# Performance work log

Hardware: AMD Instinct MI355X
Metric: run time of the kernel (lower is better)

Reference implementation:

```python
import jax, jax.numpy as jnp
import numpy as np

N_ITERS = 1000  # hardcoded in the original module
EPS = 1e-6


def setup_inputs() -> dict:
    key = jax.random.key(0)
    k1, k2 = jax.random.split(key)
    embeds = jax.random.normal(k1, (30000, 64), dtype=jnp.float32)
    # torch does t.rand(...) inside forward; we hoist it here for determinism
    init_centroids = jax.random.uniform(k2, (500, 64), dtype=jnp.float32)
    return {"embeds": embeds, "init_centroids": init_centroids}


def reference(embeds, init_centroids):
    N, D = embeds.shape
    K = init_centroids.shape[0]
    # ||e||^2 is loop-invariant; squared L2 distance expanded as
    # ||e||^2 - 2 e.c + ||c||^2 (same math as (e-c)^2.sum(-1), no [N,K,D] blowup)
    e_sq = jnp.sum(embeds * embeds, axis=1)  # [N]
    ones = jnp.ones((N, 1), dtype=embeds.dtype)

    def step(carry, _):
        cents, _, _ = carry
        c_sq = jnp.sum(cents * cents, axis=1)  # [K]
        dists = e_sq[:, None] - 2.0 * (embeds @ cents.T) + c_sq[None, :]  # [N,K]
        idxs = jnp.argmin(dists, axis=1)  # [N] int32
        sums = jax.ops.segment_sum(embeds, idxs, num_segments=K)  # [K,D]
        counts = jax.ops.segment_sum(ones, idxs, num_segments=K)  # [K,1]
        new_cents = sums / (counts + EPS)
        return (new_cents, idxs, counts), None

    init = (init_centroids,
            jnp.zeros((N,), dtype=jnp.int32),
            jnp.zeros((K, 1), dtype=embeds.dtype))
    (centroids, idxs, clust_nums), _ = jax.lax.scan(step, init, None, length=N_ITERS)
    return centroids, idxs, clust_nums
```

## Files before the change

kernel.cpp:

```cpp
#include <hip/hip_runtime.h>
#include <math.h>

#define N_PTS   30000
#define DIM     64
#define K_C     500
#define K_PAD   512
#define N_ITERS 1000

#define GRID 256
#define BLK  512

#define TM    128
#define NTM   235

#define FPSCALE 262144.0f
#define INV_FPSCALE (1.0 / 262144.0)

#define SMEM_BYTES (DIM * TM * 4 + DIM * K_PAD * 4)

#define BAR_STRIDE 32
#define BAR_REL_OFF (GRID * BAR_STRIDE)

__device__ __forceinline__ void gridbar(int* bar, int n) {
  __syncthreads();
  if (blockIdx.x == 0) {
    const int t = threadIdx.x;
    if (t >= 1 && t < GRID) {
      while (__hip_atomic_load(&bar[t * BAR_STRIDE], __ATOMIC_RELAXED,
                               __HIP_MEMORY_SCOPE_AGENT) < n)
        __builtin_amdgcn_s_sleep(2);
      __builtin_amdgcn_fence(__ATOMIC_ACQUIRE, "agent");
    }
    __syncthreads();
    if (t == 0)
      __hip_atomic_store(&bar[BAR_REL_OFF], n, __ATOMIC_RELEASE,
                         __HIP_MEMORY_SCOPE_AGENT);
  } else {
    if (threadIdx.x == 0) {
      __hip_atomic_store(&bar[blockIdx.x * BAR_STRIDE], n, __ATOMIC_RELEASE,
                         __HIP_MEMORY_SCOPE_AGENT);
      while (__hip_atomic_load(&bar[BAR_REL_OFF], __ATOMIC_RELAXED,
                               __HIP_MEMORY_SCOPE_AGENT) < n)
        __builtin_amdgcn_s_sleep(2);
      __builtin_amdgcn_fence(__ATOMIC_ACQUIRE, "agent");
    }
    __syncthreads();
  }
}

__global__ __launch_bounds__(BLK, 2)
void k_persist(const float* __restrict__ embeds,
               const float* __restrict__ cents0,
               float* __restrict__ esq,
               int* __restrict__ idx,
               int* __restrict__ gcnt,
               unsigned long long* __restrict__ acc,
               int* __restrict__ changed,
               int* __restrict__ bar,
               float* __restrict__ out) {
  extern __shared__ __align__(16) char smem[];
  float* As = (float*)smem;
  float* Bs = (float*)(smem + DIM * TM * 4);
  float* csqL   = (float*)smem;
  int*   ml_new = (int*)(smem + 2048);
  int*   ml_pl  = (int*)(smem + 2560);
  int*   ml_old = (int*)(smem + 3072);
  int*   ml_cnt = (int*)(smem + 3584);
  const int tid = threadIdx.x;
  const int bid = blockIdx.x;
  int bno = 0;

  {
    const int w = bid * 8 + (tid >> 6), d = tid & 63;
    for (int p = w; p < N_PTS; p += GRID * 8) {
      float v = embeds[(size_t)p * DIM + d];
      float s = v * v;
      #pragma unroll
      for (int m = 1; m < 64; m <<= 1) s += __shfl_xor(s, m, 64);
      if (d == 0) esq[p] = s;
    }
  }
  gridbar(bar, ++bno);

  const int m0 = bid * TM;
  const int tx = tid & 31, ty = tid >> 5;
  float esq_r[8];
  #pragma unroll
  for (int i = 0; i < 8; ++i) {
    int p = m0 + ty * 8 + i;
    esq_r[i] = (p < N_PTS) ? esq[p] : 0.f;
  }

  for (int it = 0; it < N_ITERS; ++it) {
    if (bid < NTM) {
      #pragma unroll
      for (int l = 0; l < 4; ++l) {
        int e = tid + l * BLK;
        int pl = e & 127, d4 = e >> 7;
        int p = m0 + pl;
        float4 v = make_float4(0.f, 0.f, 0.f, 0.f);
        if (p < N_PTS) v = *reinterpret_cast<const float4*>(embeds + (size_t)p * DIM + d4 * 4);
        As[(d4 * 4 + 0) * TM + pl] = v.x; As[(d4 * 4 + 1) * TM + pl] = v.y;
        As[(d4 * 4 + 2) * TM + pl] = v.z; As[(d4 * 4 + 3) * TM + pl] = v.w;
      }

      float csq_reg;
      {
        float s4[16];
        if (it == 0) {
          #pragma unroll
          for (int l = 0; l < 16; ++l) {
            float4 v = *reinterpret_cast<const float4*>(cents0 + (size_t)tid * DIM + l * 4);
            Bs[(l * 4 + 0) * K_PAD + tid] = v.x; Bs[(l * 4 + 1) * K_PAD + tid] = v.y;
            Bs[(l * 4 + 2) * K_PAD + tid] = v.z; Bs[(l * 4 + 3) * K_PAD + tid] = v.w;
            s4[l] = (v.x * v.x + v.y * v.y) + (v.z * v.z + v.w * v.w);
          }
        } else if (tid < K_C) {
          float fc = (float)gcnt[tid] + 1e-6f;
          #pragma unroll
          for (int l = 0; l < 16; ++l) {
            const unsigned long long* ap = acc + (size_t)tid * DIM + l * 4;
            longlong2 a0 = *reinterpret_cast<const longlong2*>(ap);
            longlong2 a1 = *reinterpret_cast<const longlong2*>(ap + 2);
            float n0 = (float)((double)a0.x * INV_FPSCALE) / fc;
            float n1 = (float)((double)a0.y * INV_FPSCALE) / fc;
            float n2 = (float)((double)a1.x * INV_FPSCALE) / fc;
            float n3 = (float)((double)a1.y * INV_FPSCALE) / fc;
            Bs[(l * 4 + 0) * K_PAD + tid] = n0; Bs[(l * 4 + 1) * K_PAD + tid] = n1;
            Bs[(l * 4 + 2) * K_PAD + tid] = n2; Bs[(l * 4 + 3) * K_PAD + tid] = n3;
            s4[l] = (n0 * n0 + n1 * n1) + (n2 * n2 + n3 * n3);
          }
        } else {
          #pragma unroll
          for (int l = 0; l < 16; ++l) {
            Bs[(l * 4 + 0) * K_PAD + tid] = 0.f; Bs[(l * 4 + 1) * K_PAD + tid] = 0.f;
            Bs[(l * 4 + 2) * K_PAD + tid] = 0.f; Bs[(l * 4 + 3) * K_PAD + tid] = 0.f;
            s4[l] = 0.f;
          }
        }
        float s8[8], s16[4], s32[2];
        #pragma unroll
        for (int m = 0; m < 8; ++m) s8[m] = s4[2 * m] + s4[2 * m + 1];
        #pragma unroll
        for (int m = 0; m < 4; ++m) s16[m] = s8[2 * m] + s8[2 * m + 1];
        s32[0] = s16[0] + s16[1]; s32[1] = s16[2] + s16[3];
        csq_reg = s32[0] + s32[1];
        if (tid >= K_C) csq_reg = INFINITY;
      }
      __syncthreads();

      float acc_r[8][16];
      #pragma unroll
      for (int i = 0; i < 8; ++i)
        #pragma unroll
        for (int j = 0; j < 16; ++j) acc_r[i][j] = 0.f;

      #pragma unroll 4
      for (int d = 0; d < DIM; ++d) {
        const float* ar = As + d * TM + ty * 8;
        float4 a0 = *reinterpret_cast<const float4*>(ar);
        float4 a1 = *reinterpret_cast<const float4*>(ar + 4);
        const float* br = Bs + d * K_PAD + tx * 4;
        float4 b0 = *reinterpret_cast<const float4*>(br);
        float4 b1 = *reinterpret_cast<const float4*>(br + 128);
        float4 b2 = *reinterpret_cast<const float4*>(br + 256);
        float4 b3 = *reinterpret_cast<const float4*>(br + 384);
        float av[8]  = {a0.x, a0.y, a0.z, a0.w, a1.x, a1.y, a1.z, a1.w};
        float bv[16] = {b0.x, b0.y, b0.z, b0.w, b1.x, b1.y, b1.z, b1.w,
                        b2.x, b2.y, b2.z, b2.w, b3.x, b3.y, b3.z, b3.w};
        #pragma unroll
        for (int i = 0; i < 8; ++i)
          #pragma unroll
          for (int j = 0; j < 16; ++j)
            acc_r[i][j] = fmaf(av[i], bv[j], acc_r[i][j]);
      }

      __syncthreads();
      csqL[tid] = csq_reg;
      if (tid == 0) ml_cnt[0] = 0;
      __syncthreads();

      float best[8]; int bidx[8];
      #pragma unroll
      for (int i = 0; i < 8; ++i) { best[i] = INFINITY; bidx[i] = 0; }
      #pragma unroll
      for (int q = 0; q < 4; ++q) {
        float4 cq = *reinterpret_cast<const float4*>(csqL + q * 128 + tx * 4);
        float cv[4] = {cq.x, cq.y, cq.z, cq.w};
        #pragma unroll
        for (int j = 0; j < 4; ++j) {
          int c = q * 4 + j;
          int n = q * 128 + tx * 4 + j;
          #pragma unroll
          for (int i = 0; i < 8; ++i) {
            float dd = (esq_r[i] - 2.0f * acc_r[i][c]) + cv[j];
            if (dd < best[i]) { best[i] = dd; bidx[i] = n; }
          }
        }
      }

      #pragma unroll
      for (int i = 0; i < 8; ++i) {
        float v = best[i]; int bi = bidx[i];
        #pragma unroll
        for (int s = 1; s < 32; s <<= 1) {
          float ov = __shfl_xor(v, s, 64);
          int   oi = __shfl_xor(bi, s, 64);
          if (ov < v || (ov == v && oi < bi)) { v = ov; bi = oi; }
        }
        if (tx == 0) {
          int pl = ty * 8 + i, p = m0 + pl;
          if (p < N_PTS) {
            int old = idx[p];
            if (old != bi) {
              idx[p] = bi;
              int slot = atomicAdd(ml_cnt, 1);
              ml_pl[slot] = pl; ml_old[slot] = old; ml_new[slot] = bi;
              if (slot == 0)
                __hip_atomic_store(&changed[it], 1, __ATOMIC_RELAXED,
                                   __HIP_MEMORY_SCOPE_AGENT);
            }
          }
        }
      }
      __syncthreads();

      {
        const int w8 = tid >> 6, lane = tid & 63;
        const int cnt = ml_cnt[0];
        for (int i = w8; i < cnt; i += 8) {
          int pl = ml_pl[i], old = ml_old[i], k = ml_new[i];
          float v = embeds[(size_t)(m0 + pl) * DIM + lane];
          long long iv = (long long)__float2int_rn(v * FPSCALE);
          atomicAdd(&acc[(size_t)k * DIM + lane], (unsigned long long)iv);
          if (old >= 0)
            atomicAdd(&acc[(size_t)old * DIM + lane], (unsigned long long)(-iv));
          if (lane == 0) {
            atomicAdd(&gcnt[k], 1);
            if (old >= 0) atomicAdd(&gcnt[old], -1);
          }
        }
      }
    }
    gridbar(bar, ++bno);

    if (__hip_atomic_load(&changed[it], __ATOMIC_RELAXED,
                          __HIP_MEMORY_SCOPE_AGENT) == 0)
      break;
  }

  const int tot = K_C * DIM + N_PTS + K_C;
  for (int g = bid * BLK + tid; g < tot; g += GRID * BLK) {
    float v;
    if (g < K_C * DIM) {
      int k = g >> 6;
      v = (float)((double)(long long)acc[g] * INV_FPSCALE) / ((float)gcnt[k] + 1e-6f);
    } else if (g < K_C * DIM + N_PTS) {
      v = (float)idx[g - K_C * DIM];
    } else {
      v = (float)gcnt[g - K_C * DIM - N_PTS];
    }
    out[g] = v;
  }
}

extern "C" void kernel_launch(void* const* d_in, const int* in_sizes, int n_in,
                              void* d_out, int out_size, void* d_ws, size_t ws_size,
                              hipStream_t stream) {
  const float* embeds = (const float*)d_in[0];
  const float* init_c = (const float*)d_in[1];
  float* out = (float*)d_out;

  char* w = (char*)d_ws;
  size_t off = 0;
  auto alloc = [&](size_t bytes) -> void* {
    void* p = w + off;
    off += (bytes + 255) & ~(size_t)255;
    return p;
  };
  float* cents0 = (float*)alloc((size_t)K_PAD * DIM * sizeof(float));
  float* esq    = (float*)alloc((size_t)N_PTS * sizeof(float));
  int*   idx    = (int*)  alloc((size_t)N_PTS * sizeof(int));
  int*   gcnt   = (int*)  alloc((size_t)K_C * sizeof(int));
  unsigned long long* acc =
      (unsigned long long*)alloc((size_t)K_C * DIM * sizeof(unsigned long long));
  int*   chg    = (int*)  alloc((size_t)N_ITERS * sizeof(int));
  int*   bar    = (int*)  alloc((size_t)(BAR_REL_OFF + 64) * sizeof(int));

  (void)hipFuncSetAttribute((const void*)k_persist,
                            hipFuncAttributeMaxDynamicSharedMemorySize, SMEM_BYTES);

  hipMemsetAsync(cents0, 0, (size_t)K_PAD * DIM * sizeof(float), stream);
  hipMemcpyAsync(cents0, init_c, (size_t)K_C * DIM * sizeof(float),
                 hipMemcpyDeviceToDevice, stream);
  hipMemsetAsync(gcnt, 0, (size_t)K_C * sizeof(int), stream);
  hipMemsetAsync(acc, 0, (size_t)K_C * DIM * sizeof(unsigned long long), stream);
  hipMemsetAsync(idx, 0xFF, (size_t)N_PTS * sizeof(int), stream);
  hipMemsetAsync(chg, 0, (size_t)N_ITERS * sizeof(int), stream);
  hipMemsetAsync(bar, 0, (size_t)(BAR_REL_OFF + 64) * sizeof(int), stream);

  k_persist<<<dim3(GRID), dim3(BLK), SMEM_BYTES, stream>>>(
      embeds, cents0, esq, idx, gcnt, acc, chg, bar, out);
}
```

Before: 1.944 ms.

## Recompute distances only against centroids that moved since the last iteration

Measured after the change: 1.942 ms. About the same (-0.1%).

```diff
diff --git a/kernel.cpp b/kernel.cpp
--- a/kernel.cpp
+++ b/kernel.cpp
@@ -12,6 +12,7 @@
 
 #define TM    128
 #define NTM   235
+#define DIRTY_MAX 128
 
 #define FPSCALE 262144.0f
 #define INV_FPSCALE (1.0 / 262144.0)
@@ -20,6 +21,15 @@
 
 #define BAR_STRIDE 32
 #define BAR_REL_OFF (GRID * BAR_STRIDE)
+
+__device__ __forceinline__ int SLOT(int i) { return (i / 12) * K_PAD + 500 + (i % 12); }
+#define DL(i)   SLOT(i)
+#define MLS(i)  SLOT(128 + (i))
+#define RLS(i)  SLOT(256 + (i))
+#define CNT_ML  SLOT(384)
+#define CNT_RL  SLOT(385)
+#define CNT_D   SLOT(386)
+#define RDF(i)  SLOT(387 + (i))
 
 __device__ __forceinline__ void gridbar(int* bar, int n) {
   __syncthreads();
@@ -53,22 +63,23 @@
                const float* __restrict__ cents0,
                float* __restrict__ esq,
                int* __restrict__ idx,
+               float* __restrict__ db,
                int* __restrict__ gcnt,
                unsigned long long* __restrict__ acc,
+               int* mov,
+               float* __restrict__ csq_g,
                int* __restrict__ changed,
                int* __restrict__ bar,
                float* __restrict__ out) {
   extern __shared__ __align__(16) char smem[];
   float* As = (float*)smem;
   float* Bs = (float*)(smem + DIM * TM * 4);
-  float* csqL   = (float*)smem;
-  int*   ml_new = (int*)(smem + 2048);
-  int*   ml_pl  = (int*)(smem + 2560);
-  int*   ml_old = (int*)(smem + 3072);
-  int*   ml_cnt = (int*)(smem + 3584);
+  int*   BsI = (int*)Bs;
+  float* csqL = (float*)smem;
   const int tid = threadIdx.x;
   const int bid = blockIdx.x;
   int bno = 0;
+  bool prevFull = false;
 
   {
     const int w = bid * 8 + (tid >> 6), d = tid & 63;
@@ -84,6 +95,19 @@
 
   const int m0 = bid * TM;
   const int tx = tid & 31, ty = tid >> 5;
+
+  if (bid < NTM) {
+    #pragma unroll
+    for (int l = 0; l < 4; ++l) {
+      int e = tid + l * BLK;
+      int pl = e & 127, d4 = e >> 7;
+      int p = m0 + pl;
+      float4 v = make_float4(0.f, 0.f, 0.f, 0.f);
+      if (p < N_PTS) v = *reinterpret_cast<const float4*>(embeds + (size_t)p * DIM + d4 * 4);
+      As[(d4 * 4 + 0) * TM + pl] = v.x; As[(d4 * 4 + 1) * TM + pl] = v.y;
+      As[(d4 * 4 + 2) * TM + pl] = v.z; As[(d4 * 4 + 3) * TM + pl] = v.w;
+    }
+  }
   float esq_r[8];
   #pragma unroll
   for (int i = 0; i < 8; ++i) {
@@ -91,155 +115,309 @@
     esq_r[i] = (p < N_PTS) ? esq[p] : 0.f;
   }
 
+  auto stage_col_acc = [&](int k) -> float {
+    float fc = (float)gcnt[k] + 1e-6f;
+    float s4[16];
+    #pragma unroll
+    for (int l = 0; l < 16; ++l) {
+      const unsigned long long* ap = acc + (size_t)k * DIM + l * 4;
+      longlong2 a0 = *reinterpret_cast<const longlong2*>(ap);
+      longlong2 a1 = *reinterpret_cast<const longlong2*>(ap + 2);
+      float n0 = (float)((double)a0.x * INV_FPSCALE) / fc;
+      float n1 = (float)((double)a0.y * INV_FPSCALE) / fc;
+      float n2 = (float)((double)a1.x * INV_FPSCALE) / fc;
+      float n3 = (float)((double)a1.y * INV_FPSCALE) / fc;
+      Bs[(l * 4 + 0) * K_PAD + k] = n0; Bs[(l * 4 + 1) * K_PAD + k] = n1;
+      Bs[(l * 4 + 2) * K_PAD + k] = n2; Bs[(l * 4 + 3) * K_PAD + k] = n3;
+      s4[l] = (n0 * n0 + n1 * n1) + (n2 * n2 + n3 * n3);
+    }
+    float s8[8], s16[4], s32[2];
+    #pragma unroll
+    for (int m = 0; m < 8; ++m) s8[m] = s4[2 * m] + s4[2 * m + 1];
+    #pragma unroll
+    for (int m = 0; m < 4; ++m) s16[m] = s8[2 * m] + s8[2 * m + 1];
+    s32[0] = s16[0] + s16[1]; s32[1] = s16[2] + s16[3];
+    return s32[0] + s32[1];
+  };
+
+  auto ml_append = [&](int pl, int old, int k, int it) {
+    int s = atomicAdd(&BsI[CNT_ML], 1);
+    BsI[MLS(s)] = pl | ((old + 1) << 7) | (k << 16);
+    if (s == 0)
+      __hip_atomic_store(&changed[it], 1, __ATOMIC_RELAXED,
+                         __HIP_MEMORY_SCOPE_AGENT);
+  };
+
+  auto delta_accum = [&](int it) {
+    const int w8 = tid >> 6, lane = tid & 63;
+    const int cnt = BsI[CNT_ML];
+    for (int i = w8; i < cnt; i += 8) {
+      int e = BsI[MLS(i)];
+      int pl = e & 127, old = ((e >> 7) & 511) - 1, k = e >> 16;
+      float v = embeds[(size_t)(m0 + pl) * DIM + lane];
+      long long iv = (long long)__float2int_rn(v * FPSCALE);
+      atomicAdd(&acc[(size_t)k * DIM + lane], (unsigned long long)iv);
+      if (old >= 0)
+        atomicAdd(&acc[(size_t)old * DIM + lane], (unsigned long long)(-iv));
+      if (lane == 0) {
+        atomicAdd(&gcnt[k], 1);
+        __hip_atomic_store(&mov[k], it, __ATOMIC_RELAXED, __HIP_MEMORY_SCOPE_AGENT);
+        if (old >= 0) {
+          atomicAdd(&gcnt[old], -1);
+          __hip_atomic_store(&mov[old], it, __ATOMIC_RELAXED, __HIP_MEMORY_SCOPE_AGENT);
+        }
+      }
+    }
+  };
+
   for (int it = 0; it < N_ITERS; ++it) {
     if (bid < NTM) {
-      #pragma unroll
-      for (int l = 0; l < 4; ++l) {
-        int e = tid + l * BLK;
-        int pl = e & 127, d4 = e >> 7;
-        int p = m0 + pl;
+      if (tid == 0) { BsI[CNT_ML] = 0; BsI[CNT_RL] = 0; }
+      if (it >= 2 && tid < TM) BsI[DL(tid)] = 511;
+      if (prevFull && tid < TM) {
+        int p = m0 + tid;
         float4 v = make_float4(0.f, 0.f, 0.f, 0.f);
-        if (p < N_PTS) v = *reinterpret_cast<const float4*>(embeds + (size_t)p * DIM + d4 * 4);
-        As[(d4 * 4 + 0) * TM + pl] = v.x; As[(d4 * 4 + 1) * TM + pl] = v.y;
-        As[(d4 * 4 + 2) * TM + pl] = v.z; As[(d4 * 4 + 3) * TM + pl] = v.w;
+        if (p < N_PTS) v = *reinterpret_cast<const float4*>(embeds + (size_t)p * DIM);
+        As[0 * TM + tid] = v.x; As[1 * TM + tid] = v.y;
+        As[2 * TM + tid] = v.z; As[3 * TM + tid] = v.w;
       }
-
-      float csq_reg;
-      {
-        float s4[16];
+      int D = K_C;
+      if (it >= 2) {
+        __syncthreads();
+        if (tid < 64) {
+          int cnt8 = 0;
+          #pragma unroll
+          for (int c = 0; c < 8; ++c)
+            if (mov[tid * 8 + c] >= it - 1) ++cnt8;
+          int pre = cnt8;
+          #pragma unroll
+          for (int s = 1; s < 64; s <<= 1) {
+            int o = __shfl_up(pre, s, 64);
+            if (tid >= s) pre += o;
+          }
+          int pos = pre - cnt8;
+          #pragma unroll
+          for (int c = 0; c < 8; ++c)
+            if (mov[tid * 8 + c] >= it - 1) {
+              if (pos < TM) BsI[DL(pos)] = tid * 8 + c;
+              ++pos;
+            }
+          if (tid == 63) BsI[CNT_D] = pre;
+        }
+        __syncthreads();
+        D = BsI[CNT_D];
+      }
+
+      if (D > DIRTY_MAX) {
+        float csq_reg = INFINITY;
         if (it == 0) {
-          #pragma unroll
-          for (int l = 0; l < 16; ++l) {
-            float4 v = *reinterpret_cast<const float4*>(cents0 + (size_t)tid * DIM + l * 4);
-            Bs[(l * 4 + 0) * K_PAD + tid] = v.x; Bs[(l * 4 + 1) * K_PAD + tid] = v.y;
-            Bs[(l * 4 + 2) * K_PAD + tid] = v.z; Bs[(l * 4 + 3) * K_PAD + tid] = v.w;
-            s4[l] = (v.x * v.x + v.y * v.y) + (v.z * v.z + v.w * v.w);
+          if (tid < K_C) {
+            float s4[16];
+            #pragma unroll
+            for (int l = 0; l < 16; ++l) {
+              float4 v = *reinterpret_cast<const float4*>(cents0 + (size_t)tid * DIM + l * 4);
+              Bs[(l * 4 + 0) * K_PAD + tid] = v.x; Bs[(l * 4 + 1) * K_PAD + tid] = v.y;
+              Bs[(l * 4 + 2) * K_PAD + tid] = v.z; Bs[(l * 4 + 3) * K_PAD + tid] = v.w;
+              s4[l] = (v.x * v.x + v.y * v.y) + (v.z * v.z + v.w * v.w);
+            }
+            float s8[8], s16[4], s32[2];
+            #pragma unroll
+            for (int m = 0; m < 8; ++m) s8[m] = s4[2 * m] + s4[2 * m + 1];
+            #pragma unroll
+            for (int m = 0; m < 4; ++m) s16[m] = s8[2 * m] + s8[2 * m + 1];
+            s32[0] = s16[0] + s16[1]; s32[1] = s16[2] + s16[3];
+            csq_reg = s32[0] + s32[1];
           }
         } else if (tid < K_C) {
-          float fc = (float)gcnt[tid] + 1e-6f;
-          #pragma unroll
-          for (int l = 0; l < 16; ++l) {
-            const unsigned long long* ap = acc + (size_t)tid * DIM + l * 4;
-            longlong2 a0 = *reinterpret_cast<const longlong2*>(ap);
-            longlong2 a1 = *reinterpret_cast<const longlong2*>(ap + 2);
-            float n0 = (float)((double)a0.x * INV_FPSCALE) / fc;
-            float n1 = (float)((double)a0.y * INV_FPSCALE) / fc;
-            float n2 = (float)((double)a1.x * INV_FPSCALE) / fc;
-            float n3 = (float)((double)a1.y * INV_FPSCALE) / fc;
-            Bs[(l * 4 + 0) * K_PAD + tid] = n0; Bs[(l * 4 + 1) * K_PAD + tid] = n1;
-            Bs[(l * 4 + 2) * K_PAD + tid] = n2; Bs[(l * 4 + 3) * K_PAD + tid] = n3;
-            s4[l] = (n0 * n0 + n1 * n1) + (n2 * n2 + n3 * n3);
-          }
-        } else {
-          #pragma unroll
-          for (int l = 0; l < 16; ++l) {
-            Bs[(l * 4 + 0) * K_PAD + tid] = 0.f; Bs[(l * 4 + 1) * K_PAD + tid] = 0.f;
-            Bs[(l * 4 + 2) * K_PAD + tid] = 0.f; Bs[(l * 4 + 3) * K_PAD + tid] = 0.f;
-            s4[l] = 0.f;
-          }
-        }
-        float s8[8], s16[4], s32[2];
-        #pragma unroll
-        for (int m = 0; m < 8; ++m) s8[m] = s4[2 * m] + s4[2 * m + 1];
-        #pragma unroll
-        for (int m = 0; m < 4; ++m) s16[m] = s8[2 * m] + s8[2 * m + 1];
-        s32[0] = s16[0] + s16[1]; s32[1] = s16[2] + s16[3];
-        csq_reg = s32[0] + s32[1];
-        if (tid >= K_C) csq_reg = INFINITY;
-      }
-      __syncthreads();
-
-      float acc_r[8][16];
-      #pragma unroll
-      for (int i = 0; i < 8; ++i)
-        #pragma unroll
-        for (int j = 0; j < 16; ++j) acc_r[i][j] = 0.f;
-
-      #pragma unroll 4
-      for (int d = 0; d < DIM; ++d) {
-        const float* ar = As + d * TM + ty * 8;
-        float4 a0 = *reinterpret_cast<const float4*>(ar);
-        float4 a1 = *reinterpret_cast<const float4*>(ar + 4);
-        const float* br = Bs + d * K_PAD + tx * 4;
-        float4 b0 = *reinterpret_cast<const float4*>(br);
-        float4 b1 = *reinterpret_cast<const float4*>(br + 128);
-        float4 b2 = *reinterpret_cast<const float4*>(br + 256);
-        float4 b3 = *reinterpret_cast<const float4*>(br + 384);
-        float av[8]  = {a0.x, a0.y, a0.z, a0.w, a1.x, a1.y, a1.z, a1.w};
-        float bv[16] = {b0.x, b0.y, b0.z, b0.w, b1.x, b1.y, b1.z, b1.w,
-                        b2.x, b2.y, b2.z, b2.w, b3.x, b3.y, b3.z, b3.w};
+          csq_reg = stage_col_acc(tid);
+        }
+        csq_g[tid] = csq_reg;
+        __syncthreads();
+
+        float acc_r[8][16];
         #pragma unroll
         for (int i = 0; i < 8; ++i)
           #pragma unroll
-          for (int j = 0; j < 16; ++j)
-            acc_r[i][j] = fmaf(av[i], bv[j], acc_r[i][j]);
-      }
-
-      __syncthreads();
-      csqL[tid] = csq_reg;
-      if (tid == 0) ml_cnt[0] = 0;
-      __syncthreads();
-
-      float best[8]; int bidx[8];
-      #pragma unroll
-      for (int i = 0; i < 8; ++i) { best[i] = INFINITY; bidx[i] = 0; }
-      #pragma unroll
-      for (int q = 0; q < 4; ++q) {
-        float4 cq = *reinterpret_cast<const float4*>(csqL + q * 128 + tx * 4);
-        float cv[4] = {cq.x, cq.y, cq.z, cq.w};
+          for (int j = 0; j < 16; ++j) acc_r[i][j] = 0.f;
+
+        #pragma unroll 4
+        for (int d = 0; d < DIM; ++d) {
+          const float* ar = As + d * TM + ty * 8;
+          float4 a0 = *reinterpret_cast<const float4*>(ar);
+          float4 a1 = *reinterpret_cast<const float4*>(ar + 4);
+          const float* br = Bs + d * K_PAD + tx * 4;
+          float4 b0 = *reinterpret_cast<const float4*>(br);
+          float4 b1 = *reinterpret_cast<const float4*>(br + 128);
+          float4 b2 = *reinterpret_cast<const float4*>(br + 256);
+          float4 b3 = *reinterpret_cast<const float4*>(br + 384);
+          float av[8]  = {a0.x, a0.y, a0.z, a0.w, a1.x, a1.y, a1.z, a1.w};
+          float bv[16] = {b0.x, b0.y, b0.z, b0.w, b1.x, b1.y, b1.z, b1.w,
+                          b2.x, b2.y, b2.z, b2.w, b3.x, b3.y, b3.z, b3.w};
+          #pragma unroll
+          for (int i = 0; i < 8; ++i)
+            #pragma unroll
+            for (int j = 0; j < 16; ++j)
+              acc_r[i][j] = fmaf(av[i], bv[j], acc_r[i][j]);
+        }
+
+        __syncthreads();
+        csqL[tid] = csq_reg;
+        __syncthreads();
+
+        float best[8]; int bidx[8];
+        #pragma unroll
+        for (int i = 0; i < 8; ++i) { best[i] = INFINITY; bidx[i] = 0; }
+        #pragma unroll
+        for (int q = 0; q < 4; ++q) {
+          float4 cq = *reinterpret_cast<const float4*>(csqL + q * 128 + tx * 4);
+          float cv[4] = {cq.x, cq.y, cq.z, cq.w};
+          #pragma unroll
+          for (int j = 0; j < 4; ++j) {
+            int c = q * 4 + j;
+            int n = q * 128 + tx * 4 + j;
+            #pragma unroll
+            for (int i = 0; i < 8; ++i) {
+              float dd = (esq_r[i] - 2.0f * acc_r[i][c]) + cv[j];
+              if (dd < best[i]) { best[i] = dd; bidx[i] = n; }
+            }
+          }
+        }
+        #pragma unroll
+        for (int i = 0; i < 8; ++i) {
+          float v = best[i]; int bi = bidx[i];
+          #pragma unroll
+          for (int s = 1; s < 32; s <<= 1) {
+            float ov = __shfl_xor(v, s, 64);
+            int   oi = __shfl_xor(bi, s, 64);
+            if (ov < v || (ov == v && oi < bi)) { v = ov; bi = oi; }
+          }
+          if (tx == 0) {
+            int pl = ty * 8 + i, p = m0 + pl;
+            if (p < N_PTS) {
+              db[p] = v;
+              int old = idx[p];
+              if (old != bi) { idx[p] = bi; ml_append(pl, old, bi, it); }
+            }
+          }
+        }
+        __syncthreads();
+        delta_accum(it);
+        prevFull = true;
+      } else {
+        if (tid < K_C && mov[tid] >= it - 1)
+          csq_g[tid] = stage_col_acc(tid);
+        if (tid < TM) {
+          int p = m0 + tid, dirty = 0;
+          if (p < N_PTS) {
+            int k0 = idx[p];
+            if (mov[k0] >= it - 1) {
+              dirty = 1;
+              int s = atomicAdd(&BsI[CNT_RL], 1);
+              BsI[RLS(s)] = tid | (k0 << 7);
+            }
+          }
+          BsI[RDF(tid)] = dirty;
+        }
+        __syncthreads();
+
+        const int ncol = (D + 31) >> 5;
+        int kj[4]; float csv[4];
         #pragma unroll
         for (int j = 0; j < 4; ++j) {
-          int c = q * 4 + j;
-          int n = q * 128 + tx * 4 + j;
-          #pragma unroll
-          for (int i = 0; i < 8; ++i) {
-            float dd = (esq_r[i] - 2.0f * acc_r[i][c]) + cv[j];
-            if (dd < best[i]) { best[i] = dd; bidx[i] = n; }
-          }
-        }
-      }
-
-      #pragma unroll
-      for (int i = 0; i < 8; ++i) {
-        float v = best[i]; int bi = bidx[i];
-        #pragma unroll
-        for (int s = 1; s < 32; s <<= 1) {
-          float ov = __shfl_xor(v, s, 64);
-          int   oi = __shfl_xor(bi, s, 64);
-          if (ov < v || (ov == v && oi < bi)) { v = ov; bi = oi; }
-        }
-        if (tx == 0) {
-          int pl = ty * 8 + i, p = m0 + pl;
-          if (p < N_PTS) {
-            int old = idx[p];
-            if (old != bi) {
-              idx[p] = bi;
-              int slot = atomicAdd(ml_cnt, 1);
-              ml_pl[slot] = pl; ml_old[slot] = old; ml_new[slot] = bi;
-              if (slot == 0)
-                __hip_atomic_store(&changed[it], 1, __ATOMIC_RELAXED,
-                                   __HIP_MEMORY_SCOPE_AGENT);
-            }
-          }
-        }
-      }
-      __syncthreads();
-
-      {
-        const int w8 = tid >> 6, lane = tid & 63;
-        const int cnt = ml_cnt[0];
-        for (int i = w8; i < cnt; i += 8) {
-          int pl = ml_pl[i], old = ml_old[i], k = ml_new[i];
-          float v = embeds[(size_t)(m0 + pl) * DIM + lane];
-          long long iv = (long long)__float2int_rn(v * FPSCALE);
-          atomicAdd(&acc[(size_t)k * DIM + lane], (unsigned long long)iv);
-          if (old >= 0)
-            atomicAdd(&acc[(size_t)old * DIM + lane], (unsigned long long)(-iv));
-          if (lane == 0) {
-            atomicAdd(&gcnt[k], 1);
-            if (old >= 0) atomicAdd(&gcnt[old], -1);
-          }
-        }
+          kj[j] = 511; csv[j] = INFINITY;
+          if (j < ncol) { kj[j] = BsI[DL(j * 32 + tx)]; csv[j] = csq_g[kj[j]]; }
+        }
+        float dots[8][4];
+        #pragma unroll
+        for (int i = 0; i < 8; ++i)
+          #pragma unroll
+          for (int j = 0; j < 4; ++j) dots[i][j] = 0.f;
+
+        #pragma unroll 2
+        for (int d = 0; d < DIM; ++d) {
+          const float* ar = As + d * TM + ty * 8;
+          float4 a0 = *reinterpret_cast<const float4*>(ar);
+          float4 a1 = *reinterpret_cast<const float4*>(ar + 4);
+          float av[8] = {a0.x, a0.y, a0.z, a0.w, a1.x, a1.y, a1.z, a1.w};
+          #pragma unroll
+          for (int j = 0; j < 4; ++j)
+            if (j < ncol) {
+              float b = Bs[d * K_PAD + kj[j]];
+              #pragma unroll
+              for (int i = 0; i < 8; ++i)
+                dots[i][j] = fmaf(av[i], b, dots[i][j]);
+            }
+        }
+        #pragma unroll
+        for (int i = 0; i < 8; ++i) {
+          float v = INFINITY; int bi = 511;
+          #pragma unroll
+          for (int j = 0; j < 4; ++j)
+            if (j < ncol) {
+              float dd = (esq_r[i] - 2.0f * dots[i][j]) + csv[j];
+              if (dd < v || (dd == v && kj[j] < bi)) { v = dd; bi = kj[j]; }
+            }
+          #pragma unroll
+          for (int s = 1; s < 32; s <<= 1) {
+            float ov = __shfl_xor(v, s, 64);
+            int   oi = __shfl_xor(bi, s, 64);
+            if (ov < v || (ov == v && oi < bi)) { v = ov; bi = oi; }
+          }
+          if (tx == 0) {
+            int pl = ty * 8 + i, p = m0 + pl;
+            if (p < N_PTS && !BsI[RDF(pl)]) {
+              int k0 = idx[p];
+              float dbp = db[p];
+              if (v < dbp || (v == dbp && bi < k0)) {
+                idx[p] = bi; db[p] = v; ml_append(pl, k0, bi, it);
+              }
+            }
+          }
+        }
+        __syncthreads();
+
+        {
+          const int w8 = tid >> 6, lane = tid & 63;
+          const int rcnt = BsI[CNT_RL];
+          for (int i = w8; i < rcnt; i += 8) {
+            int e = BsI[RLS(i)];
+            int pl = e & 127, k0 = e >> 7;
+            int p = m0 + pl;
+            float esq_p = esq[p];
+            float csv8[8];
+            #pragma unroll
+            for (int c = 0; c < 8; ++c) csv8[c] = csq_g[c * 64 + lane];
+            float dot[8];
+            #pragma unroll
+            for (int c = 0; c < 8; ++c) dot[c] = 0.f;
+            for (int d = 0; d < DIM; ++d) {
+              float a = As[d * TM + pl];
+              #pragma unroll
+              for (int c = 0; c < 8; ++c)
+                dot[c] = fmaf(a, Bs[d * K_PAD + c * 64 + lane], dot[c]);
+            }
+            float v = INFINITY; int bk = 511;
+            #pragma unroll
+            for (int c = 0; c < 8; ++c) {
+              float dd = (esq_p - 2.0f * dot[c]) + csv8[c];
+              int k = c * 64 + lane;
+              if (dd < v || (dd == v && k < bk)) { v = dd; bk = k; }
+            }
+            #pragma unroll
+            for (int s = 1; s < 64; s <<= 1) {
+              float ov = __shfl_xor(v, s, 64);
+              int   oi = __shfl_xor(bk, s, 64);
+              if (ov < v || (ov == v && oi < bk)) { v = ov; bk = oi; }
+            }
+            if (lane == 0) {
+              db[p] = v;
+              if (bk != k0) { idx[p] = bk; ml_append(pl, k0, bk, it); }
+            }
+          }
+        }
+        __syncthreads();
+        delta_accum(it);
+        prevFull = false;
       }
     }
     gridbar(bar, ++bno);
@@ -278,27 +456,30 @@
     off += (bytes + 255) & ~(size_t)255;
     return p;
   };
-  float* cents0 = (float*)alloc((size_t)K_PAD * DIM * sizeof(float));
+  float* cents0 = (float*)alloc((size_t)K_C * DIM * sizeof(float));
   float* esq    = (float*)alloc((size_t)N_PTS * sizeof(float));
   int*   idx    = (int*)  alloc((size_t)N_PTS * sizeof(int));
+  float* db     = (float*)alloc((size_t)N_PTS * sizeof(float));
   int*   gcnt   = (int*)  alloc((size_t)K_C * sizeof(int));
   unsigned long long* acc =
       (unsigned long long*)alloc((size_t)K_C * DIM * sizeof(unsigned long long));
+  int*   mov    = (int*)  alloc((size_t)K_PAD * sizeof(int));
+  float* csq_g  = (float*)alloc((size_t)K_PAD * sizeof(float));
   int*   chg    = (int*)  alloc((size_t)N_ITERS * sizeof(int));
   int*   bar    = (int*)  alloc((size_t)(BAR_REL_OFF + 64) * sizeof(int));
 
   (void)hipFuncSetAttribute((const void*)k_persist,
                             hipFuncAttributeMaxDynamicSharedMemorySize, SMEM_BYTES);
 
-  hipMemsetAsync(cents0, 0, (size_t)K_PAD * DIM * sizeof(float), stream);
   hipMemcpyAsync(cents0, init_c, (size_t)K_C * DIM * sizeof(float),
                  hipMemcpyDeviceToDevice, stream);
   hipMemsetAsync(gcnt, 0, (size_t)K_C * sizeof(int), stream);
   hipMemsetAsync(acc, 0, (size_t)K_C * DIM * sizeof(unsigned long long), stream);
   hipMemsetAsync(idx, 0xFF, (size_t)N_PTS * sizeof(int), stream);
+  hipMemsetAsync(mov, 0xFF, (size_t)K_PAD * sizeof(int), stream);
   hipMemsetAsync(chg, 0, (size_t)N_ITERS * sizeof(int), stream);
   hipMemsetAsync(bar, 0, (size_t)(BAR_REL_OFF + 64) * sizeof(int), stream);
 
   k_persist<<<dim3(GRID), dim3(BLK), SMEM_BYTES, stream>>>(
-      embeds, cents0, esq, idx, gcnt, acc, chg, bar, out);
+      embeds, cents0, esq, idx, db, gcnt, acc, mov, csq_g, chg, bar, out);
 }
```

## Keep embeddings tile resident and restage only moved centroids each iteration

Applied to the files above, without the earlier changes.

Measured after the change: 1.942 ms. About the same (-0.1%).

```diff
diff --git a/kernel.cpp b/kernel.cpp
--- a/kernel.cpp
+++ b/kernel.cpp
@@ -7,11 +7,10 @@
 #define K_PAD   512
 #define N_ITERS 1000
 
-#define GRID 256
-#define BLK  512
-
 #define TM    128
 #define NTM   235
+#define GRID  NTM
+#define BLK   1024
 
 #define FPSCALE 262144.0f
 #define INV_FPSCALE (1.0 / 262144.0)
@@ -20,6 +19,10 @@
 
 #define BAR_STRIDE 32
 #define BAR_REL_OFF (GRID * BAR_STRIDE)
+
+__device__ __forceinline__ int SLOT(int i) { return (i / 12) * K_PAD + 500 + (i % 12); }
+#define MLS(i)  SLOT(i)
+#define CNT_ML  SLOT(128)
 
 __device__ __forceinline__ void gridbar(int* bar, int n) {
   __syncthreads();
@@ -48,31 +51,29 @@
   }
 }
 
-__global__ __launch_bounds__(BLK, 2)
+__global__ __launch_bounds__(BLK)
 void k_persist(const float* __restrict__ embeds,
                const float* __restrict__ cents0,
                float* __restrict__ esq,
                int* __restrict__ idx,
                int* __restrict__ gcnt,
                unsigned long long* __restrict__ acc,
+               int* mov,
+               float* __restrict__ csq_g,
                int* __restrict__ changed,
                int* __restrict__ bar,
                float* __restrict__ out) {
   extern __shared__ __align__(16) char smem[];
   float* As = (float*)smem;
   float* Bs = (float*)(smem + DIM * TM * 4);
-  float* csqL   = (float*)smem;
-  int*   ml_new = (int*)(smem + 2048);
-  int*   ml_pl  = (int*)(smem + 2560);
-  int*   ml_old = (int*)(smem + 3072);
-  int*   ml_cnt = (int*)(smem + 3584);
+  int*   BsI = (int*)Bs;
   const int tid = threadIdx.x;
   const int bid = blockIdx.x;
   int bno = 0;
 
   {
-    const int w = bid * 8 + (tid >> 6), d = tid & 63;
-    for (int p = w; p < N_PTS; p += GRID * 8) {
+    const int w = bid * 16 + (tid >> 6), d = tid & 63;
+    for (int p = w; p < N_PTS; p += GRID * 16) {
       float v = embeds[(size_t)p * DIM + d];
       float s = v * v;
       #pragma unroll
@@ -83,7 +84,18 @@
   gridbar(bar, ++bno);
 
   const int m0 = bid * TM;
-  const int tx = tid & 31, ty = tid >> 5;
+  const int tx = tid & 63, ty = tid >> 6;
+
+  #pragma unroll
+  for (int l = 0; l < 2; ++l) {
+    int e = tid + l * BLK;
+    int pl = e & 127, d4 = e >> 7;
+    int p = m0 + pl;
+    float4 v = make_float4(0.f, 0.f, 0.f, 0.f);
+    if (p < N_PTS) v = *reinterpret_cast<const float4*>(embeds + (size_t)p * DIM + d4 * 4);
+    As[(d4 * 4 + 0) * TM + pl] = v.x; As[(d4 * 4 + 1) * TM + pl] = v.y;
+    As[(d4 * 4 + 2) * TM + pl] = v.z; As[(d4 * 4 + 3) * TM + pl] = v.w;
+  }
   float esq_r[8];
   #pragma unroll
   for (int i = 0; i < 8; ++i) {
@@ -92,30 +104,33 @@
   }
 
   for (int it = 0; it < N_ITERS; ++it) {
-    if (bid < NTM) {
-      #pragma unroll
-      for (int l = 0; l < 4; ++l) {
-        int e = tid + l * BLK;
-        int pl = e & 127, d4 = e >> 7;
-        int p = m0 + pl;
-        float4 v = make_float4(0.f, 0.f, 0.f, 0.f);
-        if (p < N_PTS) v = *reinterpret_cast<const float4*>(embeds + (size_t)p * DIM + d4 * 4);
-        As[(d4 * 4 + 0) * TM + pl] = v.x; As[(d4 * 4 + 1) * TM + pl] = v.y;
-        As[(d4 * 4 + 2) * TM + pl] = v.z; As[(d4 * 4 + 3) * TM + pl] = v.w;
-      }
-
-      float csq_reg;
-      {
+    if (tid == 0) BsI[CNT_ML] = 0;
+
+    if (tid < K_PAD) {
+      bool doStage;
+      if (it == 0)      doStage = true;
+      else if (it == 1) doStage = (tid < K_C);
+      else              doStage = (tid < K_C) && (mov[tid] >= it - 1);
+      if (doStage) {
         float s4[16];
         if (it == 0) {
-          #pragma unroll
-          for (int l = 0; l < 16; ++l) {
-            float4 v = *reinterpret_cast<const float4*>(cents0 + (size_t)tid * DIM + l * 4);
-            Bs[(l * 4 + 0) * K_PAD + tid] = v.x; Bs[(l * 4 + 1) * K_PAD + tid] = v.y;
-            Bs[(l * 4 + 2) * K_PAD + tid] = v.z; Bs[(l * 4 + 3) * K_PAD + tid] = v.w;
-            s4[l] = (v.x * v.x + v.y * v.y) + (v.z * v.z + v.w * v.w);
+          if (tid < K_C) {
+            #pragma unroll
+            for (int l = 0; l < 16; ++l) {
+              float4 v = *reinterpret_cast<const float4*>(cents0 + (size_t)tid * DIM + l * 4);
+              Bs[(l * 4 + 0) * K_PAD + tid] = v.x; Bs[(l * 4 + 1) * K_PAD + tid] = v.y;
+              Bs[(l * 4 + 2) * K_PAD + tid] = v.z; Bs[(l * 4 + 3) * K_PAD + tid] = v.w;
+              s4[l] = (v.x * v.x + v.y * v.y) + (v.z * v.z + v.w * v.w);
+            }
+          } else {
+            #pragma unroll
+            for (int l = 0; l < 16; ++l) {
+              Bs[(l * 4 + 0) * K_PAD + tid] = 0.f; Bs[(l * 4 + 1) * K_PAD + tid] = 0.f;
+              Bs[(l * 4 + 2) * K_PAD + tid] = 0.f; Bs[(l * 4 + 3) * K_PAD + tid] = 0.f;
+              s4[l] = 0.f;
+            }
           }
-        } else if (tid < K_C) {
+        } else {
           float fc = (float)gcnt[tid] + 1e-6f;
           #pragma unroll
           for (int l = 0; l < 16; ++l) {
@@ -130,13 +145,6 @@
             Bs[(l * 4 + 2) * K_PAD + tid] = n2; Bs[(l * 4 + 3) * K_PAD + tid] = n3;
             s4[l] = (n0 * n0 + n1 * n1) + (n2 * n2 + n3 * n3);
           }
-        } else {
-          #pragma unroll
-          for (int l = 0; l < 16; ++l) {
-            Bs[(l * 4 + 0) * K_PAD + tid] = 0.f; Bs[(l * 4 + 1) * K_PAD + tid] = 0.f;
-            Bs[(l * 4 + 2) * K_PAD + tid] = 0.f; Bs[(l * 4 + 3) * K_PAD + tid] = 0.f;
-            s4[l] = 0.f;
-          }
         }
         float s8[8], s16[4], s32[2];
         #pragma unroll
@@ -144,100 +152,98 @@
         #pragma unroll
         for (int m = 0; m < 4; ++m) s16[m] = s8[2 * m] + s8[2 * m + 1];
         s32[0] = s16[0] + s16[1]; s32[1] = s16[2] + s16[3];
-        csq_reg = s32[0] + s32[1];
-        if (tid >= K_C) csq_reg = INFINITY;
-      }
-      __syncthreads();
-
-      float acc_r[8][16];
+        float cs = s32[0] + s32[1];
+        csq_g[tid] = (tid < K_C) ? cs : INFINITY;
+      }
+    }
+    __syncthreads();
+
+    float acc_r[8][8];
+    #pragma unroll
+    for (int i = 0; i < 8; ++i)
+      #pragma unroll
+      for (int j = 0; j < 8; ++j) acc_r[i][j] = 0.f;
+
+    #pragma unroll 4
+    for (int d = 0; d < DIM; ++d) {
+      const float* ar = As + d * TM + ty * 8;
+      float4 a0 = *reinterpret_cast<const float4*>(ar);
+      float4 a1 = *reinterpret_cast<const float4*>(ar + 4);
+      const float* br = Bs + d * K_PAD + tx * 4;
+      float4 b0 = *reinterpret_cast<const float4*>(br);
+      float4 b1 = *reinterpret_cast<const float4*>(br + 256);
+      float av[8] = {a0.x, a0.y, a0.z, a0.w, a1.x, a1.y, a1.z, a1.w};
+      float bv[8] = {b0.x, b0.y, b0.z, b0.w, b1.x, b1.y, b1.z, b1.w};
       #pragma unroll
       for (int i = 0; i < 8; ++i)
         #pragma unroll
-        for (int j = 0; j < 16; ++j) acc_r[i][j] = 0.f;
-
-      #pragma unroll 4
-      for (int d = 0; d < DIM; ++d) {
-        const float* ar = As + d * TM + ty * 8;
-        float4 a0 = *reinterpret_cast<const float4*>(ar);
-        float4 a1 = *reinterpret_cast<const float4*>(ar + 4);
-        const float* br = Bs + d * K_PAD + tx * 4;
-        float4 b0 = *reinterpret_cast<const float4*>(br);
-        float4 b1 = *reinterpret_cast<const float4*>(br + 128);
-        float4 b2 = *reinterpret_cast<const float4*>(br + 256);
-        float4 b3 = *reinterpret_cast<const float4*>(br + 384);
-        float av[8]  = {a0.x, a0.y, a0.z, a0.w, a1.x, a1.y, a1.z, a1.w};
-        float bv[16] = {b0.x, b0.y, b0.z, b0.w, b1.x, b1.y, b1.z, b1.w,
-                        b2.x, b2.y, b2.z, b2.w, b3.x, b3.y, b3.z, b3.w};
+        for (int j = 0; j < 8; ++j)
+          acc_r[i][j] = fmaf(av[i], bv[j], acc_r[i][j]);
+    }
+
+    float4 c0 = *reinterpret_cast<const float4*>(csq_g + tx * 4);
+    float4 c1 = *reinterpret_cast<const float4*>(csq_g + 256 + tx * 4);
+    float cv[8] = {c0.x, c0.y, c0.z, c0.w, c1.x, c1.y, c1.z, c1.w};
+    float best[8]; int bidx[8];
+    #pragma unroll
+    for (int i = 0; i < 8; ++i) { best[i] = INFINITY; bidx[i] = 0; }
+    #pragma unroll
+    for (int g = 0; g < 2; ++g) {
+      #pragma unroll
+      for (int j = 0; j < 4; ++j) {
+        int c = g * 4 + j;
+        int n = g * 256 + tx * 4 + j;
         #pragma unroll
-        for (int i = 0; i < 8; ++i)
-          #pragma unroll
-          for (int j = 0; j < 16; ++j)
-            acc_r[i][j] = fmaf(av[i], bv[j], acc_r[i][j]);
-      }
-
-      __syncthreads();
-      csqL[tid] = csq_reg;
-      if (tid == 0) ml_cnt[0] = 0;
-      __syncthreads();
-
-      float best[8]; int bidx[8];
-      #pragma unroll
-      for (int i = 0; i < 8; ++i) { best[i] = INFINITY; bidx[i] = 0; }
-      #pragma unroll
-      for (int q = 0; q < 4; ++q) {
-        float4 cq = *reinterpret_cast<const float4*>(csqL + q * 128 + tx * 4);
-        float cv[4] = {cq.x, cq.y, cq.z, cq.w};
-        #pragma unroll
-        for (int j = 0; j < 4; ++j) {
-          int c = q * 4 + j;
-          int n = q * 128 + tx * 4 + j;
-          #pragma unroll
-          for (int i = 0; i < 8; ++i) {
-            float dd = (esq_r[i] - 2.0f * acc_r[i][c]) + cv[j];
-            if (dd < best[i]) { best[i] = dd; bidx[i] = n; }
+        for (int i = 0; i < 8; ++i) {
+          float dd = (esq_r[i] - 2.0f * acc_r[i][c]) + cv[c];
+          if (dd < best[i]) { best[i] = dd; bidx[i] = n; }
+        }
+      }
+    }
+
+    #pragma unroll
+    for (int i = 0; i < 8; ++i) {
+      float v = best[i]; int bi = bidx[i];
+      #pragma unroll
+      for (int s = 1; s < 64; s <<= 1) {
+        float ov = __shfl_xor(v, s, 64);
+        int   oi = __shfl_xor(bi, s, 64);
+        if (ov < v || (ov == v && oi < bi)) { v = ov; bi = oi; }
+      }
+      if (tx == 0) {
+        int pl = ty * 8 + i, p = m0 + pl;
+        if (p < N_PTS) {
+          int old = idx[p];
+          if (old != bi) {
+            idx[p] = bi;
+            int slot = atomicAdd(&BsI[CNT_ML], 1);
+            BsI[MLS(slot)] = pl | ((old + 1) << 7) | (bi << 16);
+            if (slot == 0)
+              __hip_atomic_store(&changed[it], 1, __ATOMIC_RELAXED,
+                                 __HIP_MEMORY_SCOPE_AGENT);
           }
         }
       }
-
-      #pragma unroll
-      for (int i = 0; i < 8; ++i) {
-        float v = best[i]; int bi = bidx[i];
-        #pragma unroll
-        for (int s = 1; s < 32; s <<= 1) {
-          float ov = __shfl_xor(v, s, 64);
-          int   oi = __shfl_xor(bi, s, 64);
-          if (ov < v || (ov == v && oi < bi)) { v = ov; bi = oi; }
-        }
-        if (tx == 0) {
-          int pl = ty * 8 + i, p = m0 + pl;
-          if (p < N_PTS) {
-            int old = idx[p];
-            if (old != bi) {
-              idx[p] = bi;
-              int slot = atomicAdd(ml_cnt, 1);
-              ml_pl[slot] = pl; ml_old[slot] = old; ml_new[slot] = bi;
-              if (slot == 0)
-                __hip_atomic_store(&changed[it], 1, __ATOMIC_RELAXED,
-                                   __HIP_MEMORY_SCOPE_AGENT);
-            }
-          }
-        }
-      }
-      __syncthreads();
-
-      {
-        const int w8 = tid >> 6, lane = tid & 63;
-        const int cnt = ml_cnt[0];
-        for (int i = w8; i < cnt; i += 8) {
-          int pl = ml_pl[i], old = ml_old[i], k = ml_new[i];
-          float v = embeds[(size_t)(m0 + pl) * DIM + lane];
-          long long iv = (long long)__float2int_rn(v * FPSCALE);
-          atomicAdd(&acc[(size_t)k * DIM + lane], (unsigned long long)iv);
-          if (old >= 0)
-            atomicAdd(&acc[(size_t)old * DIM + lane], (unsigned long long)(-iv));
-          if (lane == 0) {
-            atomicAdd(&gcnt[k], 1);
-            if (old >= 0) atomicAdd(&gcnt[old], -1);
+    }
+    __syncthreads();
+
+    {
+      const int w8 = tid >> 6, lane = tid & 63;
+      const int cnt = BsI[CNT_ML];
+      for (int i = w8; i < cnt; i += 16) {
+        int e = BsI[MLS(i)];
+        int pl = e & 127, old = ((e >> 7) & 511) - 1, k = e >> 16;
+        float v = embeds[(size_t)(m0 + pl) * DIM + lane];
+        long long iv = (long long)__float2int_rn(v * FPSCALE);
+        atomicAdd(&acc[(size_t)k * DIM + lane], (unsigned long long)iv);
+        if (old >= 0)
+          atomicAdd(&acc[(size_t)old * DIM + lane], (unsigned long long)(-iv));
+        if (lane == 0) {
+          atomicAdd(&gcnt[k], 1);
+          __hip_atomic_store(&mov[k], it, __ATOMIC_RELAXED, __HIP_MEMORY_SCOPE_AGENT);
+          if (old >= 0) {
+            atomicAdd(&gcnt[old], -1);
+            __hip_atomic_store(&mov[old], it, __ATOMIC_RELAXED, __HIP_MEMORY_SCOPE_AGENT);
           }
         }
       }
@@ -278,27 +284,29 @@
     off += (bytes + 255) & ~(size_t)255;
     return p;
   };
-  float* cents0 = (float*)alloc((size_t)K_PAD * DIM * sizeof(float));
+  float* cents0 = (float*)alloc((size_t)K_C * DIM * sizeof(float));
   float* esq    = (float*)alloc((size_t)N_PTS * sizeof(float));
   int*   idx    = (int*)  alloc((size_t)N_PTS * sizeof(int));
   int*   gcnt   = (int*)  alloc((size_t)K_C * sizeof(int));
   unsigned long long* acc =
       (unsigned long long*)alloc((size_t)K_C * DIM * sizeof(unsigned long long));
+  int*   mov    = (int*)  alloc((size_t)K_PAD * sizeof(int));
+  float* csq_g  = (float*)alloc((size_t)K_PAD * sizeof(float));
   int*   chg    = (int*)  alloc((size_t)N_ITERS * sizeof(int));
   int*   bar    = (int*)  alloc((size_t)(BAR_REL_OFF + 64) * sizeof(int));
 
   (void)hipFuncSetAttribute((const void*)k_persist,
                             hipFuncAttributeMaxDynamicSharedMemorySize, SMEM_BYTES);
 
-  hipMemsetAsync(cents0, 0, (size_t)K_PAD * DIM * sizeof(float), stream);
   hipMemcpyAsync(cents0, init_c, (size_t)K_C * DIM * sizeof(float),
                  hipMemcpyDeviceToDevice, stream);
   hipMemsetAsync(gcnt, 0, (size_t)K_C * sizeof(int), stream);
   hipMemsetAsync(acc, 0, (size_t)K_C * DIM * sizeof(unsigned long long), stream);
   hipMemsetAsync(idx, 0xFF, (size_t)N_PTS * sizeof(int), stream);
+  hipMemsetAsync(mov, 0xFF, (size_t)K_PAD * sizeof(int), stream);
   hipMemsetAsync(chg, 0, (size_t)N_ITERS * sizeof(int), stream);
   hipMemsetAsync(bar, 0, (size_t)(BAR_REL_OFF + 64) * sizeof(int), stream);
 
   k_persist<<<dim3(GRID), dim3(BLK), SMEM_BYTES, stream>>>(
-      embeds, cents0, esq, idx, gcnt, acc, chg, bar, out);
+      embeds, cents0, esq, idx, gcnt, acc, mov, csq_g, chg, bar, out);
 }
```
